# Kernel tuning notes

Hardware: AMD Instinct MI355X
Metric: run time of the kernel (lower is better)

## Reference

```python
import jax, jax.numpy as jnp
import numpy as np

B, P, C = 2, 2048, 64
SIZE = 128          # image_size
K = 8               # points_per_pixel (z-buffer depth)
RADIUS = 1.5        # in pixels
RAD_POW = 2
TAU = 1.0
BIG = 1e10          # sentinel z for pixels a point does not cover


def setup_inputs() -> dict:
    key = jax.random.key(0)
    k1, k2, k3 = jax.random.split(key, 3)
    xy = jax.random.uniform(k1, (B, P, 2), minval=-1.0, maxval=1.0)   # NDC xy
    z = jax.random.uniform(k2, (B, P, 1), minval=0.1, maxval=10.0)    # depth > 0
    pts3D = jnp.concatenate([xy, z], axis=-1)                          # [B,P,3]
    src = jax.random.normal(k3, (B, C, P), dtype=jnp.float32)          # [B,C,P]
    return {"pts3D": pts3D, "src": src}


def reference(pts3D, src):
    # --- sign flips from the torch forward: pts[:, :, :2] *= -1 ---
    pts = pts3D * jnp.array([-1.0, -1.0, 1.0], dtype=pts3D.dtype)
    px, py, pz = pts[..., 0], pts[..., 1], pts[..., 2]                 # [B,P]

    r_ndc = float(RADIUS) / float(SIZE) * 2.0

    # pixel-center NDC grid (pytorch3d convention: +x left, +y up)
    ii = jnp.arange(SIZE, dtype=pts.dtype)
    ndc = 1.0 - 2.0 * (ii + 0.5) / SIZE                                # [SIZE]

    # squared NDC distance pixel->point: [B,H,W,P]
    dx = ndc[None, None, :, None] - px[:, None, None, :]               # [B,1,W,P]
    dy = ndc[None, :, None, None] - py[:, None, None, :]               # [B,H,1,P]
    d2 = dx * dx + dy * dy                                             # [B,H,W,P]

    # rasterize_points: per pixel, K nearest-in-z points within radius
    inside = d2 <= r_ndc * r_ndc
    zkey = jnp.where(inside, pz[:, None, None, :], jnp.asarray(BIG, d2.dtype))
    neg_top, idx = jax.lax.top_k(-zkey, K)            # smallest z first, [B,H,W,K]
    valid = (-neg_top) < BIG                           # idx >= 0 equivalent

    dist = jnp.take_along_axis(d2, idx, axis=-1)       # [B,H,W,K]
    dist = dist / (r_ndc ** RAD_POW)

    # alphas = (1 - clamp(dist,0.001,1)^0.5)^tau
    alphas = (1.0 - jnp.sqrt(jnp.clip(dist, 0.001, 1.0))) ** TAU
    alphas = jnp.where(valid, alphas, 0.0)

    # alpha_composite: w_k = a_k * prod_{j<k} (1 - a_j), front-to-back
    T = jnp.cumprod(1.0 - alphas, axis=-1)
    w = alphas * jnp.concatenate([jnp.ones_like(T[..., :1]), T[..., :-1]], axis=-1)

    # gather features per batch: src [B,C,P], idx [B,H,W,K] -> [B,C,H,W,K]
    gathered = jax.vmap(lambda f, i: f[:, i])(src, idx)
    out = jnp.einsum('bchwk,bhwk->bchw', gathered, w)  # [B,C,H,W]
    return out
```

## Files before the change

kernel.cpp:

```cpp
#include <hip/hip_runtime.h>
#include <hip/hip_bf16.h>

#define BATCH 2
#define NPTS 2048
#define NCH 64
#define IMG 128
#define KTOP 8
#define BIGF 1e10f
#define CAP 128

__global__ __launch_bounds__(256) void prep(
    const float* __restrict__ pts,
    const float* __restrict__ src,
    float* __restrict__ srcT,
    float4* __restrict__ bins,
    int* __restrict__ counts) {
  const int blk = blockIdx.x;
  if (blk < 64) {
    __shared__ float tile[64][65];
    int b = blk >> 5;
    int p0 = (blk & 31) << 6;
    int tx = threadIdx.x & 63;
    int ty = threadIdx.x >> 6;
    const float* s = src + b * NCH * NPTS;
    #pragma unroll
    for (int cc = 0; cc < 64; cc += 4) {
      int c = cc + ty;
      tile[tx][c] = s[c * NPTS + p0 + tx];
    }
    __syncthreads();
    float* dT = srcT + (b * NPTS + p0) * NCH;
    #pragma unroll
    for (int pp = 0; pp < 64; pp += 4) {
      int p = pp + ty;
      dT[p * NCH + tx] = tile[p][tx];
    }
  } else {
    const int wave = threadIdx.x >> 6;
    const int lane = threadIdx.x & 63;
    const int row = ((blk - 64) << 2) + wave;
    const int b = row >> 7;
    const int h = row & 127;
    const float r_ndc = 0.0234375f;
    const float r2 = r_ndc * r_ndc;
    const float yc = 1.0f - 2.0f * (h + 0.5f) / 128.0f;
    const float* pb = pts + b * NPTS * 3;
    float4* brow = bins + row * CAP;
    int base = 0;
    for (int it = 0; it < NPTS / 64; ++it) {
      int p = (it << 6) + lane;
      float y = pb[p * 3 + 1];
      float dy = yc + y;
      bool hit = (dy * dy <= r2);
      unsigned long long mask = __ballot(hit);
      int prefix = __popcll(mask & ((1ull << lane) - 1ull));
      if (hit) {
        int pos = base + prefix;
        if (pos < CAP)
          brow[pos] = make_float4(pb[p * 3 + 0], y, pb[p * 3 + 2],
                                  __int_as_float(p));
      }
      base += __popcll(mask);
    }
    if (lane == 0) counts[row] = min(base, CAP);
  }
}

__global__ __launch_bounds__(64) void raster(
    const float4* __restrict__ bins,
    const int* __restrict__ counts,
    const float* __restrict__ srcT,
    float* __restrict__ out) {
  __shared__ float4 cand[CAP];

  const int bid = blockIdx.x;
  const int cg = bid & 3;
  const int half = (bid >> 2) & 1;
  const int h = (bid >> 3) & 127;
  const int b = bid >> 10;
  const int lane = threadIdx.x;

  const int row = (b << 7) + h;
  const int cnt = min(counts[row], CAP);
  const float4* grow = bins + row * CAP;
  for (int j = lane; j < cnt; j += 64) cand[j] = grow[j];
  __syncthreads();

  const float r_ndc = 0.0234375f;
  const float r2 = r_ndc * r_ndc;
  const float yc = 1.0f - 2.0f * (h + 0.5f) / 128.0f;
  const int w = (half << 6) + lane;
  const float xc = 1.0f - 2.0f * (w + 0.5f) / 128.0f;

  float bz[KTOP], bd[KTOP];
  int bp[KTOP];
  #pragma unroll
  for (int k = 0; k < KTOP; ++k) { bz[k] = BIGF; bd[k] = 0.f; bp[k] = 0; }

  for (int j = 0; j < cnt; ++j) {
    float4 c4 = cand[j];
    float dx = xc + c4.x;
    float dyy = yc + c4.y;
    float d2 = dx * dx + dyy * dyy;
    if (d2 <= r2) {
      float cz = c4.z, cd = d2;
      int cp = __float_as_int(c4.w);
      #pragma unroll
      for (int s = 0; s < KTOP; ++s) {
        bool lt = (cz < bz[s]);
        float tz = bz[s], td = bd[s];
        int tp = bp[s];
        if (lt) { bz[s] = cz; bd[s] = cd; bp[s] = cp;
                  cz = tz; cd = td; cp = tp; }
      }
    }
  }

  float wgt[KTOP];
  float T = 1.0f;
  const float inv_r2 = 1.0f / r2;
  #pragma unroll
  for (int k = 0; k < KTOP; ++k) {
    float alpha = 0.0f;
    if (bz[k] < BIGF) {
      float dist = bd[k] * inv_r2;
      dist = fminf(fmaxf(dist, 0.001f), 1.0f);
      alpha = 1.0f - sqrtf(dist);
    }
    wgt[k] = alpha * T;
    T *= (1.0f - alpha);
  }

  const float* sb = srcT + (size_t)b * NPTS * NCH + cg * 16;
  float4 acc0 = {0,0,0,0}, acc1 = {0,0,0,0}, acc2 = {0,0,0,0}, acc3 = {0,0,0,0};
  #pragma unroll
  for (int k = 0; k < KTOP; ++k) {
    const float4* fr = (const float4*)(sb + (size_t)bp[k] * NCH);
    float wk = wgt[k];
    float4 v0 = fr[0], v1 = fr[1], v2 = fr[2], v3 = fr[3];
    acc0.x += wk * v0.x; acc0.y += wk * v0.y; acc0.z += wk * v0.z; acc0.w += wk * v0.w;
    acc1.x += wk * v1.x; acc1.y += wk * v1.y; acc1.z += wk * v1.z; acc1.w += wk * v1.w;
    acc2.x += wk * v2.x; acc2.y += wk * v2.y; acc2.z += wk * v2.z; acc2.w += wk * v2.w;
    acc3.x += wk * v3.x; acc3.y += wk * v3.y; acc3.z += wk * v3.z; acc3.w += wk * v3.w;
  }

  float* ob = out + (((size_t)b * NCH + cg * 16) * IMG + h) * IMG + w;
  const int S = IMG * IMG;
  ob[0 * S] = acc0.x;  ob[1 * S] = acc0.y;  ob[2 * S] = acc0.z;  ob[3 * S] = acc0.w;
  ob[4 * S] = acc1.x;  ob[5 * S] = acc1.y;  ob[6 * S] = acc1.z;  ob[7 * S] = acc1.w;
  ob[8 * S] = acc2.x;  ob[9 * S] = acc2.y;  ob[10 * S] = acc2.z; ob[11 * S] = acc2.w;
  ob[12 * S] = acc3.x; ob[13 * S] = acc3.y; ob[14 * S] = acc3.z; ob[15 * S] = acc3.w;
}

extern "C" void kernel_launch(void* const* d_in, const int* in_sizes, int n_in,
                              void* d_out, int out_size, void* d_ws, size_t ws_size,
                              hipStream_t stream) {
  const float* pts = (const float*)d_in[0];
  const float* src = (const float*)d_in[1];
  float* out = (float*)d_out;

  char* ws = (char*)d_ws;
  float* srcT = (float*)ws;
  float4* bins = (float4*)(ws + (size_t)BATCH * NPTS * NCH * 4);
  int* counts = (int*)(ws + (size_t)BATCH * NPTS * NCH * 4 +
                       (size_t)BATCH * IMG * CAP * 16);

  prep<<<128, 256, 0, stream>>>(pts, src, srcT, bins, counts);
  raster<<<BATCH * IMG * 2 * 4, 64, 0, stream>>>(bins, counts, srcT, out);
}
```

Before: 86.02 us.

## Fuse row binning and feature transpose into a single raster kernel

Removes the separate prep kernel. Each raster block now bins the candidate points for its own image row directly into shared memory, and gathers features straight from the original [B,C,P] src layout instead of a transposed copy. This drops one launch, the workspace round-trip and the transpose. In exchange, every block redoes the full 2048-point scan, which is repeated 8 times per row, and the feature gathers become strided scalar loads instead of float4 rows.

```diff
diff --git a/kernel.cpp b/kernel.cpp
--- a/kernel.cpp
+++ b/kernel.cpp
@@ -9,67 +9,9 @@
 #define BIGF 1e10f
 #define CAP 128
 
-__global__ __launch_bounds__(256) void prep(
+__global__ __launch_bounds__(64) void raster_mega(
     const float* __restrict__ pts,
     const float* __restrict__ src,
-    float* __restrict__ srcT,
-    float4* __restrict__ bins,
-    int* __restrict__ counts) {
-  const int blk = blockIdx.x;
-  if (blk < 64) {
-    __shared__ float tile[64][65];
-    int b = blk >> 5;
-    int p0 = (blk & 31) << 6;
-    int tx = threadIdx.x & 63;
-    int ty = threadIdx.x >> 6;
-    const float* s = src + b * NCH * NPTS;
-    #pragma unroll
-    for (int cc = 0; cc < 64; cc += 4) {
-      int c = cc + ty;
-      tile[tx][c] = s[c * NPTS + p0 + tx];
-    }
-    __syncthreads();
-    float* dT = srcT + (b * NPTS + p0) * NCH;
-    #pragma unroll
-    for (int pp = 0; pp < 64; pp += 4) {
-      int p = pp + ty;
-      dT[p * NCH + tx] = tile[p][tx];
-    }
-  } else {
-    const int wave = threadIdx.x >> 6;
-    const int lane = threadIdx.x & 63;
-    const int row = ((blk - 64) << 2) + wave;
-    const int b = row >> 7;
-    const int h = row & 127;
-    const float r_ndc = 0.0234375f;
-    const float r2 = r_ndc * r_ndc;
-    const float yc = 1.0f - 2.0f * (h + 0.5f) / 128.0f;
-    const float* pb = pts + b * NPTS * 3;
-    float4* brow = bins + row * CAP;
-    int base = 0;
-    for (int it = 0; it < NPTS / 64; ++it) {
-      int p = (it << 6) + lane;
-      float y = pb[p * 3 + 1];
-      float dy = yc + y;
-      bool hit = (dy * dy <= r2);
-      unsigned long long mask = __ballot(hit);
-      int prefix = __popcll(mask & ((1ull << lane) - 1ull));
-      if (hit) {
-        int pos = base + prefix;
-        if (pos < CAP)
-          brow[pos] = make_float4(pb[p * 3 + 0], y, pb[p * 3 + 2],
-                                  __int_as_float(p));
-      }
-      base += __popcll(mask);
-    }
-    if (lane == 0) counts[row] = min(base, CAP);
-  }
-}
-
-__global__ __launch_bounds__(64) void raster(
-    const float4* __restrict__ bins,
-    const int* __restrict__ counts,
-    const float* __restrict__ srcT,
     float* __restrict__ out) {
   __shared__ float4 cand[CAP];
 
@@ -80,15 +22,31 @@
   const int b = bid >> 10;
   const int lane = threadIdx.x;
 
-  const int row = (b << 7) + h;
-  const int cnt = min(counts[row], CAP);
-  const float4* grow = bins + row * CAP;
-  for (int j = lane; j < cnt; j += 64) cand[j] = grow[j];
-  __syncthreads();
-
   const float r_ndc = 0.0234375f;
   const float r2 = r_ndc * r_ndc;
   const float yc = 1.0f - 2.0f * (h + 0.5f) / 128.0f;
+
+  const float* pb = pts + b * NPTS * 3;
+  int base = 0;
+  for (int it = 0; it < NPTS / 64; ++it) {
+    int p = (it << 6) + lane;
+    float y = pb[p * 3 + 1];
+    float dy = yc + y;
+    bool hit = (dy * dy <= r2);
+    unsigned long long mask = __ballot(hit);
+    if (mask) {
+      if (hit) {
+        int pos = base + __popcll(mask & ((1ull << lane) - 1ull));
+        if (pos < CAP)
+          cand[pos] = make_float4(pb[p * 3 + 0], y, pb[p * 3 + 2],
+                                  __int_as_float(p));
+      }
+      base += __popcll(mask);
+    }
+  }
+  __syncthreads();
+  const int cnt = min(base, CAP);
+
   const int w = (half << 6) + lane;
   const float xc = 1.0f - 2.0f * (w + 0.5f) / 128.0f;
 
@@ -131,25 +89,24 @@
     T *= (1.0f - alpha);
   }
 
-  const float* sb = srcT + (size_t)b * NPTS * NCH + cg * 16;
-  float4 acc0 = {0,0,0,0}, acc1 = {0,0,0,0}, acc2 = {0,0,0,0}, acc3 = {0,0,0,0};
+  const float* sb = src + ((size_t)b * NCH + cg * 16) * NPTS;
+  float acc[16];
+  #pragma unroll
+  for (int c = 0; c < 16; ++c) acc[c] = 0.0f;
   #pragma unroll
   for (int k = 0; k < KTOP; ++k) {
-    const float4* fr = (const float4*)(sb + (size_t)bp[k] * NCH);
     float wk = wgt[k];
-    float4 v0 = fr[0], v1 = fr[1], v2 = fr[2], v3 = fr[3];
-    acc0.x += wk * v0.x; acc0.y += wk * v0.y; acc0.z += wk * v0.z; acc0.w += wk * v0.w;
-    acc1.x += wk * v1.x; acc1.y += wk * v1.y; acc1.z += wk * v1.z; acc1.w += wk * v1.w;
-    acc2.x += wk * v2.x; acc2.y += wk * v2.y; acc2.z += wk * v2.z; acc2.w += wk * v2.w;
-    acc3.x += wk * v3.x; acc3.y += wk * v3.y; acc3.z += wk * v3.z; acc3.w += wk * v3.w;
+    int p = bp[k];
+    #pragma unroll
+    for (int c = 0; c < 16; ++c)
+      acc[c] += wk * sb[c * NPTS + p];
   }
 
   float* ob = out + (((size_t)b * NCH + cg * 16) * IMG + h) * IMG + w;
   const int S = IMG * IMG;
-  ob[0 * S] = acc0.x;  ob[1 * S] = acc0.y;  ob[2 * S] = acc0.z;  ob[3 * S] = acc0.w;
-  ob[4 * S] = acc1.x;  ob[5 * S] = acc1.y;  ob[6 * S] = acc1.z;  ob[7 * S] = acc1.w;
-  ob[8 * S] = acc2.x;  ob[9 * S] = acc2.y;  ob[10 * S] = acc2.z; ob[11 * S] = acc2.w;
-  ob[12 * S] = acc3.x; ob[13 * S] = acc3.y; ob[14 * S] = acc3.z; ob[15 * S] = acc3.w;
+  #pragma unroll
+  for (int c = 0; c < 16; ++c)
+    ob[c * S] = acc[c];
 }
 
 extern "C" void kernel_launch(void* const* d_in, const int* in_sizes, int n_in,
@@ -159,12 +116,5 @@
   const float* src = (const float*)d_in[1];
   float* out = (float*)d_out;
 
-  char* ws = (char*)d_ws;
-  float* srcT = (float*)ws;
-  float4* bins = (float4*)(ws + (size_t)BATCH * NPTS * NCH * 4);
-  int* counts = (int*)(ws + (size_t)BATCH * NPTS * NCH * 4 +
-                       (size_t)BATCH * IMG * CAP * 16);
-
-  prep<<<128, 256, 0, stream>>>(pts, src, srcT, bins, counts);
-  raster<<<BATCH * IMG * 2 * 4, 64, 0, stream>>>(bins, counts, srcT, out);
+  raster_mega<<<BATCH * IMG * 2 * 4, 64, 0, stream>>>(pts, src, out);
 }
```

Result: faster. 83.55 us (-2.9%).

## Stage candidate features in LDS and merge channel-group blocks into one

Applied to the files above, without the earlier changes.

Merges the four channel-group blocks per half-row into a single 256-thread block. The block cooperatively gathers the features of all row candidates into padded shared memory, and the compositing step reads from LDS by candidate index instead of doing scattered global loads per pixel. The aim is to cut redundant global feature traffic. In exchange it adds a gather of all candidates' features, even those not in any pixel's top-k, and a larger shared-memory footprint.

```diff
diff --git a/kernel.cpp b/kernel.cpp
--- a/kernel.cpp
+++ b/kernel.cpp
@@ -8,6 +8,7 @@
 #define KTOP 8
 #define BIGF 1e10f
 #define CAP 128
+#define FPITCH 68
 
 __global__ __launch_bounds__(256) void prep(
     const float* __restrict__ pts,
@@ -66,36 +67,47 @@
   }
 }
 
-__global__ __launch_bounds__(64) void raster(
+__global__ __launch_bounds__(256) void raster(
     const float4* __restrict__ bins,
     const int* __restrict__ counts,
     const float* __restrict__ srcT,
     float* __restrict__ out) {
   __shared__ float4 cand[CAP];
+  __shared__ float feat[CAP * FPITCH];
 
   const int bid = blockIdx.x;
-  const int cg = bid & 3;
-  const int half = (bid >> 2) & 1;
-  const int h = (bid >> 3) & 127;
-  const int b = bid >> 10;
-  const int lane = threadIdx.x;
+  const int half = bid & 1;
+  const int h = (bid >> 1) & 127;
+  const int b = bid >> 8;
+  const int tid = threadIdx.x;
 
   const int row = (b << 7) + h;
   const int cnt = min(counts[row], CAP);
   const float4* grow = bins + row * CAP;
-  for (int j = lane; j < cnt; j += 64) cand[j] = grow[j];
+  for (int j = tid; j < cnt; j += 256) cand[j] = grow[j];
+  __syncthreads();
+
+  const float* sT = srcT + (size_t)b * NPTS * NCH;
+  for (int t = tid; t < cnt * NCH; t += 256) {
+    int j = t >> 6;
+    int c = t & 63;
+    int p = __float_as_int(cand[j].w);
+    feat[j * FPITCH + c] = sT[(size_t)p * NCH + c];
+  }
+  if (cnt == 0 && tid < NCH) feat[tid] = 0.0f;
   __syncthreads();
 
   const float r_ndc = 0.0234375f;
   const float r2 = r_ndc * r_ndc;
   const float yc = 1.0f - 2.0f * (h + 0.5f) / 128.0f;
+  const int lane = tid & 63;
   const int w = (half << 6) + lane;
   const float xc = 1.0f - 2.0f * (w + 0.5f) / 128.0f;
 
   float bz[KTOP], bd[KTOP];
-  int bp[KTOP];
+  int bj[KTOP];
   #pragma unroll
-  for (int k = 0; k < KTOP; ++k) { bz[k] = BIGF; bd[k] = 0.f; bp[k] = 0; }
+  for (int k = 0; k < KTOP; ++k) { bz[k] = BIGF; bd[k] = 0.f; bj[k] = 0; }
 
   for (int j = 0; j < cnt; ++j) {
     float4 c4 = cand[j];
@@ -104,14 +116,14 @@
     float d2 = dx * dx + dyy * dyy;
     if (d2 <= r2) {
       float cz = c4.z, cd = d2;
-      int cp = __float_as_int(c4.w);
+      int cj = j;
       #pragma unroll
       for (int s = 0; s < KTOP; ++s) {
         bool lt = (cz < bz[s]);
         float tz = bz[s], td = bd[s];
-        int tp = bp[s];
-        if (lt) { bz[s] = cz; bd[s] = cd; bp[s] = cp;
-                  cz = tz; cd = td; cp = tp; }
+        int tj = bj[s];
+        if (lt) { bz[s] = cz; bd[s] = cd; bj[s] = cj;
+                  cz = tz; cd = td; cj = tj; }
       }
     }
   }
@@ -131,25 +143,34 @@
     T *= (1.0f - alpha);
   }
 
-  const float* sb = srcT + (size_t)b * NPTS * NCH + cg * 16;
-  float4 acc0 = {0,0,0,0}, acc1 = {0,0,0,0}, acc2 = {0,0,0,0}, acc3 = {0,0,0,0};
+  const int cq0 = (tid >> 6) * 4;
+  const float4* f4 = (const float4*)feat;
+  float4 acc[4];
+  #pragma unroll
+  for (int q = 0; q < 4; ++q) acc[q] = make_float4(0.f, 0.f, 0.f, 0.f);
   #pragma unroll
   for (int k = 0; k < KTOP; ++k) {
-    const float4* fr = (const float4*)(sb + (size_t)bp[k] * NCH);
     float wk = wgt[k];
-    float4 v0 = fr[0], v1 = fr[1], v2 = fr[2], v3 = fr[3];
-    acc0.x += wk * v0.x; acc0.y += wk * v0.y; acc0.z += wk * v0.z; acc0.w += wk * v0.w;
-    acc1.x += wk * v1.x; acc1.y += wk * v1.y; acc1.z += wk * v1.z; acc1.w += wk * v1.w;
-    acc2.x += wk * v2.x; acc2.y += wk * v2.y; acc2.z += wk * v2.z; acc2.w += wk * v2.w;
-    acc3.x += wk * v3.x; acc3.y += wk * v3.y; acc3.z += wk * v3.z; acc3.w += wk * v3.w;
+    int base = bj[k] * (FPITCH / 4) + cq0;
+    #pragma unroll
+    for (int q = 0; q < 4; ++q) {
+      float4 v = f4[base + q];
+      acc[q].x += wk * v.x;
+      acc[q].y += wk * v.y;
+      acc[q].z += wk * v.z;
+      acc[q].w += wk * v.w;
+    }
   }
 
-  float* ob = out + (((size_t)b * NCH + cg * 16) * IMG + h) * IMG + w;
+  float* ob = out + (((size_t)b * NCH + cq0 * 4) * IMG + h) * IMG + w;
   const int S = IMG * IMG;
-  ob[0 * S] = acc0.x;  ob[1 * S] = acc0.y;  ob[2 * S] = acc0.z;  ob[3 * S] = acc0.w;
-  ob[4 * S] = acc1.x;  ob[5 * S] = acc1.y;  ob[6 * S] = acc1.z;  ob[7 * S] = acc1.w;
-  ob[8 * S] = acc2.x;  ob[9 * S] = acc2.y;  ob[10 * S] = acc2.z; ob[11 * S] = acc2.w;
-  ob[12 * S] = acc3.x; ob[13 * S] = acc3.y; ob[14 * S] = acc3.z; ob[15 * S] = acc3.w;
+  #pragma unroll
+  for (int q = 0; q < 4; ++q) {
+    ob[(q * 4 + 0) * S] = acc[q].x;
+    ob[(q * 4 + 1) * S] = acc[q].y;
+    ob[(q * 4 + 2) * S] = acc[q].z;
+    ob[(q * 4 + 3) * S] = acc[q].w;
+  }
 }
 
 extern "C" void kernel_launch(void* const* d_in, const int* in_sizes, int n_in,
@@ -166,5 +187,5 @@
                        (size_t)BATCH * IMG * CAP * 16);
 
   prep<<<128, 256, 0, stream>>>(pts, src, srcT, bins, counts);
-  raster<<<BATCH * IMG * 2 * 4, 64, 0, stream>>>(bins, counts, srcT, out);
+  raster<<<BATCH * IMG * 2, 256, 0, stream>>>(bins, counts, srcT, out);
 }
```

New measurement: 86.85 us. No clear change (+1.0%).
